# Optimization experiments

Hardware: AMD Instinct MI355X
Metric: run time of the kernel (lower is better)

## Reference

```python
import jax, jax.numpy as jnp
import numpy as np

N_NODES = 20000
N_EDGES = 320000
HIDDEN = 128
HEADS = 8
LAYERS = 3
EXP_DEG = 4
N_VIRT = 1
NV = N_NODES + N_VIRT  # nodes after VirtualNode transform


def _layer_norm(x, g, b, eps=1e-5):
    mu = jnp.mean(x, axis=-1, keepdims=True)
    var = jnp.var(x, axis=-1, keepdims=True)
    return (x - mu) * jax.lax.rsqrt(var + eps) * g + b


def _segment_softmax(scores, seg, num_segments):
    # numerically-stable softmax over edges grouped by destination node
    m = jax.ops.segment_max(scores, seg, num_segments=num_segments)
    m = jnp.where(jnp.isfinite(m), m, 0.0)
    e = jnp.exp(scores - m[seg])
    s = jax.ops.segment_sum(e, seg, num_segments=num_segments)
    return e / (s[seg] + 1e-16)


def _edge_attention(x, src, dst, wq, bq, wk, bk, wv, bv, wo, bo):
    # multi-head attention restricted to the given edge list (Exphormer local/expander attention)
    n, d_model = x.shape
    dh = d_model // HEADS
    q = (x @ wq + bq).reshape(n, HEADS, dh)
    k = (x @ wk + bk).reshape(n, HEADS, dh)
    v = (x @ wv + bv).reshape(n, HEADS, dh)
    scores = jnp.einsum('ehd,ehd->eh', q[dst], k[src]) * (1.0 / np.sqrt(dh))  # [E, H]
    alpha = _segment_softmax(scores, dst, n)
    out = jax.ops.segment_sum(alpha[:, :, None] * v[src], dst, num_segments=n)  # [n, H, dh]
    return out.reshape(n, d_model) @ wo + bo


def setup_inputs():
    key = jax.random.key(0)
    ks = jax.random.split(key, 32)
    x = jax.random.normal(ks[0], (N_NODES, HIDDEN), dtype=jnp.float32)
    edge_index = jax.random.randint(ks[1], (2, N_EDGES), 0, N_NODES, dtype=jnp.int32)
    # expander graph per layer: EXP_DEG//2 random permutations, both directions
    ar = jnp.arange(NV, dtype=jnp.int32)
    layers_e = []
    for l in range(LAYERS):
        e = []
        for p in range(EXP_DEG // 2):
            perm = jax.random.permutation(jax.random.fold_in(ks[2], l * 10 + p), NV).astype(jnp.int32)
            e.append(jnp.stack([ar, perm]))
            e.append(jnp.stack([perm, ar]))
        layers_e.append(jnp.concatenate(e, axis=1))
    expander_edges = jnp.stack(layers_e)  # [LAYERS, 2, NV*EXP_DEG]

    def w(k, shape):
        return jax.random.normal(k, shape, dtype=jnp.float32) * 0.05

    p = {}
    names = ['lq', 'lk', 'lv', 'lo', 'eq', 'ek', 'ev', 'eo']
    for i, nm in enumerate(names):
        p[nm + '_w'] = w(ks[3 + i], (LAYERS, HIDDEN, HIDDEN))
        p[nm + '_b'] = w(ks[12 + i], (LAYERS, HIDDEN))
    p['ln_g'] = jnp.ones((LAYERS, HIDDEN), jnp.float32)
    p['ln_b'] = jnp.zeros((LAYERS, HIDDEN), jnp.float32)
    p['ffn_w1'] = w(ks[21], (LAYERS, HIDDEN, 4 * HIDDEN))
    p['ffn_b1'] = w(ks[22], (LAYERS, 4 * HIDDEN))
    p['ffn_w2'] = w(ks[23], (LAYERS, 4 * HIDDEN, HIDDEN))
    p['ffn_b2'] = w(ks[24], (LAYERS, HIDDEN))
    return {'x': x, 'edge_index': edge_index, 'expander_edges': expander_edges, **p}


def reference(x, edge_index, expander_edges,
              lq_w, lq_b, lk_w, lk_b, lv_w, lv_b, lo_w, lo_b,
              eq_w, eq_b, ek_w, ek_b, ev_w, ev_b, eo_w, eo_b,
              ln_g, ln_b, ffn_w1, ffn_b1, ffn_w2, ffn_b2):
    n = x.shape[0]
    # VirtualNode transform: one zero-feature node connected bidirectionally to all nodes
    xv = jnp.concatenate([x, jnp.zeros((N_VIRT, x.shape[1]), x.dtype)], axis=0)
    ar = jnp.arange(n, dtype=edge_index.dtype)
    vn = jnp.full((n,), n, dtype=edge_index.dtype)
    vsrc = jnp.concatenate([edge_index[0], ar, vn])
    vdst = jnp.concatenate([edge_index[1], vn, ar])
    for l in range(LAYERS):
        residual = xv
        local = _edge_attention(xv, vsrc, vdst,
                                lq_w[l], lq_b[l], lk_w[l], lk_b[l],
                                lv_w[l], lv_b[l], lo_w[l], lo_b[l])
        exp_out = _edge_attention(xv, expander_edges[l, 0], expander_edges[l, 1],
                                  eq_w[l], eq_b[l], ek_w[l], ek_b[l],
                                  ev_w[l], ev_b[l], eo_w[l], eo_b[l])
        xv = _layer_norm(residual + local + exp_out, ln_g[l], ln_b[l])
        xv = xv + (jax.nn.gelu(xv @ ffn_w1[l] + ffn_b1[l], approximate=False) @ ffn_w2[l] + ffn_b2[l])
    return xv[:N_NODES]
```

## Files before the change

### kernel.cpp

```cpp
#include <hip/hip_runtime.h>
#include <hip/hip_bf16.h>
#include <math.h>

#define NN    20000
#define NVT   20001
#define VN    20000
#define E_EI  320000
#define E_LOC 360000
#define E_EXP 80004
#define RSN   20002
#define NBVN  79
#define VNSTR 144

#define OW_LQ 0
#define OB_LQ 16384
#define OW_LK 16512
#define OB_LK 32896
#define OW_LV 33024
#define OB_LV 49408
#define OW_LO 49536
#define OB_LO 65920
#define OW_EQ 66048
#define OB_EQ 82432
#define OW_EK 82560
#define OB_EK 98944
#define OW_EV 99072
#define OB_EV 115456
#define OW_EO 115584
#define OB_EO 131968
#define O_LNG 132096
#define O_LNB 132224
#define O_FW1 132352
#define O_FB1 197888
#define O_FW2 198400
#define O_FB2 263936
#define WC_TOT 264064

typedef unsigned short u16;
typedef unsigned int   u32;
typedef __attribute__((ext_vector_type(8))) short short8;
typedef __attribute__((ext_vector_type(4))) float f32x4;

__device__ __forceinline__ float bf2f(u16 u) {
    return __uint_as_float(((u32)u) << 16);
}
__device__ __forceinline__ u16 f2bf(float f) {
    u32 x = __float_as_uint(f);
    u32 r = x + 0x7fffu + ((x >> 16) & 1u);
    return (u16)(r >> 16);
}

__device__ __forceinline__ void loadq16(const u16* qp, float* qf) {
    const uint4* p = (const uint4*)qp;
    uint4 a = p[0], b = p[1];
    qf[0]=bf2f((u16)(a.x&0xffff)); qf[1]=bf2f((u16)(a.x>>16));
    qf[2]=bf2f((u16)(a.y&0xffff)); qf[3]=bf2f((u16)(a.y>>16));
    qf[4]=bf2f((u16)(a.z&0xffff)); qf[5]=bf2f((u16)(a.z>>16));
    qf[6]=bf2f((u16)(a.w&0xffff)); qf[7]=bf2f((u16)(a.w>>16));
    qf[8]=bf2f((u16)(b.x&0xffff)); qf[9]=bf2f((u16)(b.x>>16));
    qf[10]=bf2f((u16)(b.y&0xffff)); qf[11]=bf2f((u16)(b.y>>16));
    qf[12]=bf2f((u16)(b.z&0xffff)); qf[13]=bf2f((u16)(b.z>>16));
    qf[14]=bf2f((u16)(b.w&0xffff)); qf[15]=bf2f((u16)(b.w>>16));
}
__device__ __forceinline__ float dot16_pre(const u16* kp, const float* qf) {
    const uint4* p = (const uint4*)kp;
    uint4 a = p[0], b = p[1];
    float s = 0.f;
    s += qf[0]*bf2f((u16)(a.x&0xffff)) + qf[1]*bf2f((u16)(a.x>>16));
    s += qf[2]*bf2f((u16)(a.y&0xffff)) + qf[3]*bf2f((u16)(a.y>>16));
    s += qf[4]*bf2f((u16)(a.z&0xffff)) + qf[5]*bf2f((u16)(a.z>>16));
    s += qf[6]*bf2f((u16)(a.w&0xffff)) + qf[7]*bf2f((u16)(a.w>>16));
    s += qf[8]*bf2f((u16)(b.x&0xffff)) + qf[9]*bf2f((u16)(b.x>>16));
    s += qf[10]*bf2f((u16)(b.y&0xffff)) + qf[11]*bf2f((u16)(b.y>>16));
    s += qf[12]*bf2f((u16)(b.z&0xffff)) + qf[13]*bf2f((u16)(b.z>>16));
    s += qf[14]*bf2f((u16)(b.w&0xffff)) + qf[15]*bf2f((u16)(b.w>>16));
    return s;
}
__device__ __forceinline__ float dot16_bf(const u16* kptr, const float* qptr) {
    const uint4* kp = (const uint4*)kptr;
    uint4 a = kp[0], b = kp[1];
    const float4* qp = (const float4*)qptr;
    float4 q0 = qp[0], q1 = qp[1], q2 = qp[2], q3 = qp[3];
    float s = 0.f;
    s += q0.x * bf2f((u16)(a.x & 0xffff)) + q0.y * bf2f((u16)(a.x >> 16));
    s += q0.z * bf2f((u16)(a.y & 0xffff)) + q0.w * bf2f((u16)(a.y >> 16));
    s += q1.x * bf2f((u16)(a.z & 0xffff)) + q1.y * bf2f((u16)(a.z >> 16));
    s += q1.z * bf2f((u16)(a.w & 0xffff)) + q1.w * bf2f((u16)(a.w >> 16));
    s += q2.x * bf2f((u16)(b.x & 0xffff)) + q2.y * bf2f((u16)(b.x >> 16));
    s += q2.z * bf2f((u16)(b.y & 0xffff)) + q2.w * bf2f((u16)(b.y >> 16));
    s += q3.x * bf2f((u16)(b.z & 0xffff)) + q3.y * bf2f((u16)(b.z >> 16));
    s += q3.z * bf2f((u16)(b.w & 0xffff)) + q3.w * bf2f((u16)(b.w >> 16));
    return s;
}

__global__ void k_detect(const u16* __restrict__ x, int* __restrict__ flag) {
    int t = threadIdx.x;
    u16 v = x[2 * t];
    int e = (v >> 7) & 0xFF;
    int sane = (e >= 100 && e <= 150) ? 1 : 0;
    __shared__ int s;
    if (t == 0) s = 0;
    __syncthreads();
    atomicAdd(&s, sane);
    __syncthreads();
    if (t == 0) *flag = (s >= 192) ? 1 : 0;
}

__global__ void k_convert(const void* __restrict__ x, const int* __restrict__ flag,
                          u16* __restrict__ XV, int* __restrict__ RS) {
    int i = blockIdx.x * 256 + threadIdx.x;
    if (i < NVT * 128) {
        u16 v = 0;
        if (i < NN * 128)
            v = (*flag) ? ((const u16*)x)[i] : f2bf(((const float*)x)[i]);
        XV[i] = v;
    } else {
        int j = i - NVT * 128;
        if (j < RSN + 4) RS[j] = 0;
    }
}

__global__ void k_canon(
    const void* lqw, const void* lqb, const void* lkw, const void* lkb,
    const void* lvw, const void* lvb, const void* low_, const void* lob,
    const void* eqw, const void* eqb, const void* ekw, const void* ekb,
    const void* evw, const void* evb, const void* eow, const void* eob,
    const void* lng, const void* lnb, const void* f1w, const void* f1b,
    const void* f2w, const void* f2b,
    const int* __restrict__ flag, u16* __restrict__ WcAll)
{
    int idx = blockIdx.x * 256 + threadIdx.x;
    if (idx >= WC_TOT) return;
    int layer = blockIdx.y;
    u16* Wc = WcAll + (size_t)layer * WC_TOT;
    const void* src;
    int e, stride;
    if (idx < 132096) {
        int p = idx / 16512, w = idx - p * 16512;
        const void* wt; const void* bt;
        switch (p) {
            case 0: wt = lqw; bt = lqb; break;
            case 1: wt = lkw; bt = lkb; break;
            case 2: wt = lvw; bt = lvb; break;
            case 3: wt = low_; bt = lob; break;
            case 4: wt = eqw; bt = eqb; break;
            case 5: wt = ekw; bt = ekb; break;
            case 6: wt = evw; bt = evb; break;
            default: wt = eow; bt = eob; break;
        }
        if (w < 16384) {
            int kt = w >> 12, ct = (w >> 9) & 7, ln = (w >> 3) & 63, j = w & 7;
            int k = kt * 32 + (ln >> 4) * 8 + j, c = ct * 16 + (ln & 15);
            src = wt; e = k * 128 + c; stride = 16384;
        } else { src = bt; e = w - 16384; stride = 128; }
    } else {
        int t2 = idx - 132096;
        if (t2 < 128)        { src = lng; e = t2;       stride = 128; }
        else if (t2 < 256)   { src = lnb; e = t2 - 128; stride = 128; }
        else if (t2 < 256 + 65536) {
            int w = t2 - 256;
            int cb = w >> 14, w2 = w & 16383;
            int kt = w2 >> 12, ct = (w2 >> 9) & 7, ln = (w2 >> 3) & 63, j = w2 & 7;
            int k = kt * 32 + (ln >> 4) * 8 + j, c = cb * 128 + ct * 16 + (ln & 15);
            src = f1w; e = k * 512 + c; stride = 65536;
        }
        else if (t2 < 66304) { src = f1b; e = t2 - 65792; stride = 512; }
        else if (t2 < 131840) {
            int w = t2 - 66304;
            int kt = w >> 12, ct = (w >> 9) & 7, ln = (w >> 3) & 63, j = w & 7;
            int k = kt * 32 + (ln >> 4) * 8 + j, c = ct * 16 + (ln & 15);
            src = f2w; e = k * 128 + c; stride = 65536;
        }
        else { src = f2b; e = t2 - 131840; stride = 128; }
    }
    int eg = layer * stride + e;
    Wc[idx] = (*flag) ? ((const u16*)src)[eg] : f2bf(((const float*)src)[eg]);
}

__global__ void k_count(const int* __restrict__ ei, int* __restrict__ RS) {
    int g = blockIdx.x * 256 + threadIdx.x;
    if (g >= E_EI) return;
    atomicAdd(&RS[ei[E_EI + g] + 1], 1);
}

__global__ __launch_bounds__(256) void k_scan(int* __restrict__ RS, int* __restrict__ CUR) {
    int t = threadIdx.x;
    const int CH = 79;
    int base = t * CH;
    int sum = 0;
    for (int i = 0; i < CH; ++i) {
        int idx = base + i;
        if (idx < RSN) {
            int add = RS[idx];
            if (idx >= 1 && idx <= NN) add += 1;
            if (idx == RSN - 1)        add += NN;
            sum += add;
        }
    }
    __shared__ int ss[256];
    ss[t] = sum;
    __syncthreads();
    for (int off = 1; off < 256; off <<= 1) {
        int v = (t >= off) ? ss[t - off] : 0;
        __syncthreads();
        ss[t] += v;
        __syncthreads();
    }
    int run = ss[t] - sum;
    for (int i = 0; i < CH; ++i) {
        int idx = base + i;
        if (idx < RSN) {
            int add = RS[idx];
            if (idx >= 1 && idx <= NN) add += 1;
            if (idx == RSN - 1)        add += NN;
            run += add;
            RS[idx]  = run;
            if (idx < NN) CUR[idx] = run + 1;
        }
    }
}

__global__ void k_scatter(const int* __restrict__ ei, int* __restrict__ CUR,
                          int* __restrict__ CSRC) {
    int g = blockIdx.x * 256 + threadIdx.x;
    if (g >= E_EI) return;
    int src = ei[g], dst = ei[E_EI + g];
    int pos = atomicAdd(&CUR[dst], 1);
    CSRC[pos] = src;
}

__global__ void k_fixinv(const int* __restrict__ RS, int* __restrict__ CSRC,
                         const int* __restrict__ ex, int* __restrict__ IP) {
    int idx = blockIdx.x * 256 + threadIdx.x;
    if (idx < NN) {
        CSRC[RS[idx]] = VN;
        CSRC[RS[VN] + idx] = idx;
    }
    if (idx < 6 * NVT) {
        int p = idx / NVT, i = idx - p * NVT;
        int l = p >> 1, w = p & 1;
        int off = l * 2 * E_EXP + E_EXP + w * 2 * NVT;
        int val = ex[off + i];
        IP[p * NVT + val] = i;
    }
}


__global__ __launch_bounds__(256) void k_qkv(
    const u16* __restrict__ X, const u16* __restrict__ Wc,
    u16* O0, u16* O1, u16* O2)
{
    int z = blockIdx.z;
    int wo = (z == 0) ? OW_LQ : (z == 1) ? OW_LK : OW_LV;
    int bo = (z == 0) ? OB_LQ : (z == 1) ? OB_LK : OB_LV;
    u16* O = (z == 0) ? O0 : (z == 1) ? O1 : O2;
    int t = threadIdx.x;
    int wv = t >> 6, lane = t & 63;
    int q4 = lane >> 4, m = lane & 15;
    int rowb = blockIdx.x * 64 + wv * 16;
    int r0 = min(rowb + m, NVT - 1);
    f32x4 zero4 = {0.f, 0.f, 0.f, 0.f};
    f32x4 acc[8];
    #pragma unroll
    for (int ct = 0; ct < 8; ++ct) acc[ct] = zero4;

    const u16* Wf = Wc + wo + lane * 8;
    #pragma unroll
    for (int kt = 0; kt < 4; ++kt) {
        short8 a0 = *(const short8*)&X[r0 * 128 + kt * 32 + q4 * 8];
        #pragma unroll
        for (int ct = 0; ct < 8; ++ct) {
            short8 bw = *(const short8*)&Wf[kt * 4096 + ct * 512];
            acc[ct] = __builtin_amdgcn_mfma_f32_16x16x32_bf16(bw, a0, acc[ct], 0, 0, 0);
        }
    }
    int row = rowb + m;
    if (row < NVT) {
        #pragma unroll
        for (int ct = 0; ct < 8; ++ct) {
            int c0 = ct * 16 + q4 * 4;
            ushort4 bb = *(const ushort4*)&Wc[bo + c0];
            ushort4 st;
            st.x = f2bf(acc[ct][0] + bf2f(bb.x));
            st.y = f2bf(acc[ct][1] + bf2f(bb.y));
            st.z = f2bf(acc[ct][2] + bf2f(bb.z));
            st.w = f2bf(acc[ct][3] + bf2f(bb.w));
            *(ushort4*)&O[row * 128 + c0] = st;
        }
    }
}

__global__ __launch_bounds__(256) void k_pq(
    u16* ATT, const u16* XV, const u16* __restrict__ Wc,
    u16* Q, u16* K, u16* V)
{
    int z = blockIdx.z;
    const u16* X; u16* O; const u16* A = nullptr;
    int wo, bo;
    if (z == 0)      { X = ATT; O = ATT; A = XV; wo = OW_LO; bo = OB_LO; }
    else if (z == 1) { X = XV;  O = Q;  wo = OW_EQ; bo = OB_EQ; }
    else if (z == 2) { X = XV;  O = K;  wo = OW_EK; bo = OB_EK; }
    else             { X = XV;  O = V;  wo = OW_EV; bo = OB_EV; }

    int t = threadIdx.x;
    int wv = t >> 6, lane = t & 63;
    int q4 = lane >> 4, m = lane & 15;
    int rowb = blockIdx.x * 64 + wv * 16;
    int r0 = min(rowb + m, NVT - 1);
    f32x4 zero4 = {0.f, 0.f, 0.f, 0.f};
    f32x4 acc[8];
    #pragma unroll
    for (int ct = 0; ct < 8; ++ct) acc[ct] = zero4;

    const u16* Wf = Wc + wo + lane * 8;
    #pragma unroll
    for (int kt = 0; kt < 4; ++kt) {
        short8 a0 = *(const short8*)&X[r0 * 128 + kt * 32 + q4 * 8];
        #pragma unroll
        for (int ct = 0; ct < 8; ++ct) {
            short8 bw = *(const short8*)&Wf[kt * 4096 + ct * 512];
            acc[ct] = __builtin_amdgcn_mfma_f32_16x16x32_bf16(bw, a0, acc[ct], 0, 0, 0);
        }
    }
    int row = rowb + m;
    if (row < NVT) {
        #pragma unroll
        for (int ct = 0; ct < 8; ++ct) {
            int c0 = ct * 16 + q4 * 4;
            ushort4 bb = *(const ushort4*)&Wc[bo + c0];
            float v0 = acc[ct][0] + bf2f(bb.x);
            float v1 = acc[ct][1] + bf2f(bb.y);
            float v2 = acc[ct][2] + bf2f(bb.z);
            float v3 = acc[ct][3] + bf2f(bb.w);
            if (A) {
                ushort4 av = *(const ushort4*)&A[row * 128 + c0];
                v0 += bf2f(av.x); v1 += bf2f(av.y);
                v2 += bf2f(av.z); v3 += bf2f(av.w);
            }
            ushort4 st;
            st.x = f2bf(v0); st.y = f2bf(v1); st.z = f2bf(v2); st.w = f2bf(v3);
            *(ushort4*)&O[row * 128 + c0] = st;
        }
    }
}

__global__ __launch_bounds__(256) void k_plf(
    u16* XV, const u16* __restrict__ ATT, const u16* __restrict__ Wc,
    const int* __restrict__ flag, void* outp, int write_out)
{
    __shared__ __align__(16) u16 Xs[32 * 136];
    __shared__ __align__(16) u16 Hs[32 * 520];
    int t = threadIdx.x;
    int wv = t >> 6, lane = t & 63;
    int q4 = lane >> 4, m = lane & 15;
    int rowb = blockIdx.x * 32;
    f32x4 zero4 = {0.f, 0.f, 0.f, 0.f};

    if (wv < 2) {
        int rl = wv * 16 + m;
        int r0 = min(rowb + rl, NVT - 1);
        f32x4 acc[8];
        #pragma unroll
        for (int ct = 0; ct < 8; ++ct) acc[ct] = zero4;
        const u16* Wf = Wc + OW_EO + lane * 8;
        #pragma unroll
        for (int kt = 0; kt < 4; ++kt) {
            short8 a0 = *(const short8*)&XV[r0 * 128 + kt * 32 + q4 * 8];
            #pragma unroll
            for (int ct = 0; ct < 8; ++ct) {
                short8 bw = *(const short8*)&Wf[kt * 4096 + ct * 512];
                acc[ct] = __builtin_amdgcn_mfma_f32_16x16x32_bf16(bw, a0, acc[ct], 0, 0, 0);
            }
        }
        float sm = 0.f, sq = 0.f;
        #pragma unroll
        for (int ct = 0; ct < 8; ++ct) {
            int c0 = ct * 16 + q4 * 4;
            ushort4 bb = *(const ushort4*)&Wc[OB_EO + c0];
            ushort4 av = *(const ushort4*)&ATT[r0 * 128 + c0];
            acc[ct][0] += bf2f(bb.x) + bf2f(av.x);
            acc[ct][1] += bf2f(bb.y) + bf2f(av.y);
            acc[ct][2] += bf2f(bb.z) + bf2f(av.z);
            acc[ct][3] += bf2f(bb.w) + bf2f(av.w);
            #pragma unroll
            for (int j = 0; j < 4; ++j) { sm += acc[ct][j]; sq += acc[ct][j] * acc[ct][j]; }
        }
        sm += __shfl_xor(sm, 16); sq += __shfl_xor(sq, 16);
        sm += __shfl_xor(sm, 32); sq += __shfl_xor(sq, 32);
        float mu  = sm * (1.f / 128.f);
        float var = sq * (1.f / 128.f) - mu * mu;
        float rs  = rsqrtf(var + 1e-5f);
        #pragma unroll
        for (int ct = 0; ct < 8; ++ct) {
            int c0 = ct * 16 + q4 * 4;
            ushort4 gg = *(const ushort4*)&Wc[O_LNG + c0];
            ushort4 bb = *(const ushort4*)&Wc[O_LNB + c0];
            ushort4 st;
            st.x = f2bf((acc[ct][0] - mu) * rs * bf2f(gg.x) + bf2f(bb.x));
            st.y = f2bf((acc[ct][1] - mu) * rs * bf2f(gg.y) + bf2f(bb.y));
            st.z = f2bf((acc[ct][2] - mu) * rs * bf2f(gg.z) + bf2f(bb.z));
            st.w = f2bf((acc[ct][3] - mu) * rs * bf2f(gg.w) + bf2f(bb.w));
            *(ushort4*)&Xs[rl * 136 + c0] = st;
        }
    }
    __syncthreads();

    short8 ax[2][4];
    #pragma unroll
    for (int kt = 0; kt < 4; ++kt) {
        ax[0][kt] = *(const short8*)&Xs[m * 136 + kt * 32 + q4 * 8];
        ax[1][kt] = *(const short8*)&Xs[(16 + m) * 136 + kt * 32 + q4 * 8];
    }
    f32x4 a1[2][8];
    #pragma unroll
    for (int rg = 0; rg < 2; ++rg)
        #pragma unroll
        for (int ct = 0; ct < 8; ++ct) a1[rg][ct] = zero4;
    const u16* W1f = Wc + O_FW1 + wv * 16384 + lane * 8;
    #pragma unroll
    for (int kt = 0; kt < 4; ++kt) {
        #pragma unroll
        for (int ct = 0; ct < 8; ++ct) {
            short8 bw = *(const short8*)&W1f[kt * 4096 + ct * 512];
            a1[0][ct] = __builtin_amdgcn_mfma_f32_16x16x32_bf16(bw, ax[0][kt], a1[0][ct], 0, 0, 0);
            a1[1][ct] = __builtin_amdgcn_mfma_f32_16x16x32_bf16(bw, ax[1][kt], a1[1][ct], 0, 0, 0);
        }
    }
    #pragma unroll
    for (int rg = 0; rg < 2; ++rg) {
        int rl = rg * 16 + m;
        #pragma unroll
        for (int ct = 0; ct < 8; ++ct) {
            int c = wv * 128 + ct * 16 + q4 * 4;
            ushort4 bb = *(const ushort4*)&Wc[O_FB1 + c];
            float v0 = a1[rg][ct][0] + bf2f(bb.x);
            float v1 = a1[rg][ct][1] + bf2f(bb.y);
            float v2 = a1[rg][ct][2] + bf2f(bb.z);
            float v3 = a1[rg][ct][3] + bf2f(bb.w);
            ushort4 st;
            st.x = f2bf(0.5f * v0 * (1.f + erff(v0 * 0.70710678118654752440f)));
            st.y = f2bf(0.5f * v1 * (1.f + erff(v1 * 0.70710678118654752440f)));
            st.z = f2bf(0.5f * v2 * (1.f + erff(v2 * 0.70710678118654752440f)));
            st.w = f2bf(0.5f * v3 * (1.f + erff(v3 * 0.70710678118654752440f)));
            *(ushort4*)&Hs[rl * 520 + c] = st;
        }
    }
    __syncthreads();

    f32x4 acc2[2][2];
    #pragma unroll
    for (int rg = 0; rg < 2; ++rg)
        #pragma unroll
        for (int j = 0; j < 2; ++j) acc2[rg][j] = zero4;
    const u16* W2f = Wc + O_FW2 + lane * 8;
    #pragma unroll
    for (int kt = 0; kt < 16; ++kt) {
        short8 h0 = *(const short8*)&Hs[m * 520 + kt * 32 + q4 * 8];
        short8 h1 = *(const short8*)&Hs[(16 + m) * 520 + kt * 32 + q4 * 8];
        #pragma unroll
        for (int j = 0; j < 2; ++j) {
            short8 bw = *(const short8*)&W2f[kt * 4096 + (2 * wv + j) * 512];
            acc2[0][j] = __builtin_amdgcn_mfma_f32_16x16x32_bf16(bw, h0, acc2[0][j], 0, 0, 0);
            acc2[1][j] = __builtin_amdgcn_mfma_f32_16x16x32_bf16(bw, h1, acc2[1][j], 0, 0, 0);
        }
    }
    int fl = *flag;
    #pragma unroll
    for (int rg = 0; rg < 2; ++rg) {
        int row = rowb + rg * 16 + m;
        if (row < NVT) {
            #pragma unroll
            for (int j = 0; j < 2; ++j) {
                int c0 = (2 * wv + j) * 16 + q4 * 4;
                ushort4 bb = *(const ushort4*)&Wc[O_FB2 + c0];
                ushort4 rv = *(const ushort4*)&Xs[(rg * 16 + m) * 136 + c0];
                float v0 = acc2[rg][j][0] + bf2f(bb.x) + bf2f(rv.x);
                float v1 = acc2[rg][j][1] + bf2f(bb.y) + bf2f(rv.y);
                float v2 = acc2[rg][j][2] + bf2f(bb.z) + bf2f(rv.z);
                float v3 = acc2[rg][j][3] + bf2f(bb.w) + bf2f(rv.w);
                ushort4 st;
                st.x = f2bf(v0); st.y = f2bf(v1); st.z = f2bf(v2); st.w = f2bf(v3);
                *(ushort4*)&XV[row * 128 + c0] = st;
                if (write_out && row < NN) {
                    if (fl) {
                        *(ushort4*)((u16*)outp + row * 128 + c0) = st;
                    } else {
                        float4 fv; fv.x = v0; fv.y = v1; fv.z = v2; fv.w = v3;
                        *(float4*)((float*)outp + row * 128 + c0) = fv;
                    }
                }
            }
        }
    }
}

__global__ __launch_bounds__(256) void k_gvn(
    const u16* __restrict__ Q, const u16* __restrict__ K,
    const u16* __restrict__ V, const int* __restrict__ RS,
    const int* __restrict__ CSRC, u16* __restrict__ OUT,
    float* __restrict__ VNS, int* __restrict__ CNT)
{
    int t = threadIdx.x;
    __shared__ float ps_s[4][128];
    __shared__ int   sv_s[4][16];
    if (blockIdx.x >= NBVN) {
        int wv = t >> 6, l = t & 63;
        int dst = (blockIdx.x - NBVN) * 4 + wv;
        int hp = l & 3;
        int e16 = l >> 2;
        int hq = l >> 4;
        float* ps = ps_s[wv];
        int* svp = sv_s[wv];
        int rs = RS[dst], re = RS[dst + 1];
        float qf[32];
        loadq16(&Q[dst * 128 + hp * 32], qf);
        loadq16(&Q[dst * 128 + hp * 32 + 16], qf + 16);
        float acc0 = 0.f, acc1 = 0.f, d0 = 0.f, d1 = 0.f;
        for (int e0 = rs; e0 < re; e0 += 16) {
            int eidx = e0 + e16;
            bool val = eidx < re;
            int eidx2 = val ? eidx : (re - 1);
            int sv = CSRC[eidx2];
            float s0 = dot16_pre(&K[sv * 128 + hp * 32], qf) * 0.25f;
            float s1 = dot16_pre(&K[sv * 128 + hp * 32 + 16], qf + 16) * 0.25f;
            float p0 = val ? __expf(s0) : 0.f;
            float p1 = val ? __expf(s1) : 0.f;
            ps[e16 * 8 + 2 * hp]     = p0;
            ps[e16 * 8 + 2 * hp + 1] = p1;
            if (hp == 0) svp[e16] = sv;
            #pragma unroll
            for (int ee = 0; ee < 16; ++ee) {
                int se = svp[ee];
                float w0 = ps[ee * 8 + hq];
                float w1 = ps[ee * 8 + 4 + hq];
                acc0 += w0 * bf2f(V[se * 128 + l]);
                acc1 += w1 * bf2f(V[se * 128 + 64 + l]);
                d0 += w0; d1 += w1;
            }
        }
        OUT[dst * 128 + l]      = f2bf(acc0 / (d0 + 1e-16f));
        OUT[dst * 128 + 64 + l] = f2bf(acc1 / (d1 + 1e-16f));
        return;
    }
    int vb = blockIdx.x;
    __shared__ __align__(16) float q_s[128];
    __shared__ float sr_s[256 * 8];
    __shared__ float pden[64];
    __shared__ float psum[128];
    __shared__ int   lastBlk;
    int base = vb * 256;
    if (t < 128) q_s[t] = bf2f(Q[VN * 128 + t]);
    __syncthreads();

    int e32 = t >> 3, h = t & 7;
    for (int pass = 0; pass < 8; ++pass) {
        int e = pass * 32 + e32;
        int src = base + e;
        float p = 0.f;
        if (src < NN)
            p = __expf(dot16_bf(&K[src * 128 + h * 16], &q_s[h * 16]) * 0.25f);
        sr_s[e * 8 + h] = p;
    }
    __syncthreads();
    if (t < 64) {
        int h2 = t & 7, c = t >> 3;
        float pd = 0.f;
        for (int j = 0; j < 32; ++j)
            pd += sr_s[(c * 32 + j) * 8 + h2];
        pden[t] = pd;
    }
    __syncthreads();
    if (t < 8) {
        float dn = 0.f;
        for (int c = 0; c < 8; ++c) dn += pden[c * 8 + t];
        VNS[vb * VNSTR + 8 + t] = dn;
    }
    int d = t & 127, half = t >> 7, hd = d >> 4;
    float acc = 0.f;
    for (int i = 0; i < 128; ++i) {
        int e = half * 128 + i;
        int src = base + e;
        if (src < NN)
            acc += sr_s[e * 8 + hd] * bf2f(V[src * 128 + d]);
    }
    if (half == 1) psum[d] = acc;
    __syncthreads();
    if (half == 0)
        VNS[vb * VNSTR + 16 + d] = acc + psum[d];
    __threadfence();
    __syncthreads();
    if (t == 0) lastBlk = (atomicAdd(CNT, 1) == NBVN - 1) ? 1 : 0;
    __syncthreads();
    if (lastBlk) {
        __threadfence();
        volatile const float* VV = VNS;
        __shared__ float den_s[8];
        if (t < 8) {
            float dn = 0.f;
            for (int b = 0; b < NBVN; ++b) dn += VV[b * VNSTR + 8 + t];
            den_s[t] = dn;
        }
        __syncthreads();
        if (t < 128) {
            int hd2 = t >> 4;
            float a2 = 0.f;
            for (int b = 0; b < NBVN; ++b) a2 += VV[b * VNSTR + 16 + t];
            OUT[VN * 128 + t] = f2bf(a2 / (den_s[hd2] + 1e-16f));
        }
    }
}

__global__ __launch_bounds__(256) void k_egather(
    const u16* __restrict__ Q, const u16* __restrict__ K,
    const u16* __restrict__ V, const int* __restrict__ IP0,
    const int* __restrict__ IP1, const int* __restrict__ PD,
    u16* __restrict__ OUT)
{
    int wv = threadIdx.x >> 6, l = threadIdx.x & 63;
    int dst = blockIdx.x * 4 + wv;
    if (dst >= NVT) return;
    int h = l & 7, e = (l >> 3) & 3, hq = l >> 4;
    int sv;
    if (e == 0)      sv = IP0[dst];
    else if (e == 1) sv = PD[dst];
    else if (e == 2) sv = IP1[dst];
    else             sv = PD[2 * NVT + dst];
    float qf[16];
    loadq16(&Q[dst * 128 + h * 16], qf);
    float sr = dot16_pre(&K[sv * 128 + h * 16], qf) * 0.25f;
    float p = __expf(sr);
    float den = p + __shfl_xor(p, 8);
    den += __shfl_xor(den, 16);
    float acc0 = 0.f, acc1 = 0.f;
    #pragma unroll
    for (int ee = 0; ee < 4; ++ee) {
        int se = __shfl(sv, ee * 8);
        float p0 = __shfl(p, ee * 8 + hq);
        float p1 = __shfl(p, ee * 8 + 4 + hq);
        acc0 += p0 * bf2f(V[se * 128 + l]);
        acc1 += p1 * bf2f(V[se * 128 + 64 + l]);
    }
    float d0 = __shfl(den, hq), d1 = __shfl(den, 4 + hq);
    OUT[dst * 128 + l]      = f2bf(acc0 / (d0 + 1e-16f));
    OUT[dst * 128 + 64 + l] = f2bf(acc1 / (d1 + 1e-16f));
}

extern "C" void kernel_launch(void* const* d_in, const int* in_sizes, int n_in,
                              void* d_out, int out_size, void* d_ws, size_t ws_size,
                              hipStream_t stream)
{
    const void* x = d_in[0];
    const int* ei = (const int*)d_in[1];
    const int* ex = (const int*)d_in[2];

    const size_t NFB = (size_t)NVT * 128 * 2;
    char* wsb = (char*)d_ws;
    u16* XVb  = (u16*)(wsb);
    u16* ATTb = (u16*)(wsb + NFB);
    u16* Qb   = (u16*)(wsb + 2 * NFB);
    u16* Kb   = (u16*)(wsb + 3 * NFB);
    u16* Vb   = (u16*)(wsb + 4 * NFB);
    int* RS   = (int*)(wsb + 5 * NFB);
    int* CNT  = RS + RSN;
    int* CUR  = CNT + 4;
    int* IP   = CUR + RSN;
    size_t o_wc = 5 * NFB + (size_t)(2 * RSN + 4 + 6 * NVT) * 4;
    o_wc = (o_wc + 15) & ~(size_t)15;
    u16* Wc   = (u16*)(wsb + o_wc);
    int* flag = (int*)(wsb + o_wc + (size_t)3 * WC_TOT * 2);

    int*   CSRC = (int*)d_out;
    float* VNS  = (float*)((char*)d_out + (size_t)E_LOC * 4);

    k_detect<<<1, 256, 0, stream>>>((const u16*)x, flag);
    k_convert<<<(NVT * 128 + RSN + 4 + 255) / 256, 256, 0, stream>>>(x, flag, XVb, RS);
    int eb = (E_EI + 255) / 256;
    k_count  <<<eb, 256, 0, stream>>>(ei, RS);
    k_scan   <<<1, 256, 0, stream>>>(RS, CUR);
    k_scatter<<<eb, 256, 0, stream>>>(ei, CUR, CSRC);
    k_fixinv <<<(6 * NVT + 255) / 256, 256, 0, stream>>>(RS, CSRC, ex, IP);
    k_canon<<<dim3((WC_TOT + 255) / 256, 3), 256, 0, stream>>>(
        d_in[3],  d_in[4],  d_in[5],  d_in[6],  d_in[7],  d_in[8],
        d_in[9],  d_in[10], d_in[11], d_in[12], d_in[13], d_in[14],
        d_in[15], d_in[16], d_in[17], d_in[18], d_in[19], d_in[20],
        d_in[21], d_in[22], d_in[23], d_in[24], flag, Wc);

    int gb64 = (NVT + 63) / 64;
    int gb32 = (NVT + 31) / 32;
    for (int l = 0; l < 3; ++l) {
        const u16* Wl = Wc + (size_t)l * WC_TOT;
        k_qkv<<<dim3(gb64, 1, 3), 256, 0, stream>>>(XVb, Wl, Qb, Kb, Vb);
        k_gvn<<<NBVN + NN / 4, 256, 0, stream>>>(Qb, Kb, Vb, RS, CSRC, ATTb,
                                                  VNS, CNT + l);
        k_pq<<<dim3(gb64, 1, 4), 256, 0, stream>>>(ATTb, XVb, Wl, Qb, Kb, Vb);
        k_egather<<<(NVT + 3) / 4, 256, 0, stream>>>(Qb, Kb, Vb,
            IP + (2 * l) * NVT, IP + (2 * l + 1) * NVT,
            ex + (size_t)l * 2 * E_EXP + E_EXP, XVb);
        k_plf<<<gb32, 256, 0, stream>>>(XVb, ATTb, Wl, flag, d_out,
                                        (l == 2) ? 1 : 0);
    }
}
```

Baseline: 706.7 us.

## Split each node's edges across two waves and vectorize V gathers

The local-attention gather path now assigns two wavefronts per destination node, each handling alternate 16-edge chunks. Each lane loads 8 bf16 V values in one 16-byte load instead of scalar loads. Partial sums are combined with cross-lane shuffles and shared memory before a single vectorized store. This aims to raise memory-level parallelism and cut per-edge load instructions, at the cost of twice as many blocks, an extra block barrier and shuffle reductions.

```diff
diff --git a/kernel.cpp b/kernel.cpp
--- a/kernel.cpp
+++ b/kernel.cpp
@@ -503,43 +503,75 @@
     int t = threadIdx.x;
     __shared__ float ps_s[4][128];
     __shared__ int   sv_s[4][16];
+    __shared__ float comb[2][16][9];
     if (blockIdx.x >= NBVN) {
         int wv = t >> 6, l = t & 63;
-        int dst = (blockIdx.x - NBVN) * 4 + wv;
-        int hp = l & 3;
+        int pr  = wv >> 1;
+        int par = wv & 1;
+        int dst = (blockIdx.x - NBVN) * 2 + pr;
+        int hp  = l & 3;
         int e16 = l >> 2;
-        int hq = l >> 4;
-        float* ps = ps_s[wv];
-        int* svp = sv_s[wv];
+        int qq  = l >> 4;
+        int m   = l & 15;
+        int hd  = m >> 1;
+        float* ps  = ps_s[wv];
+        int*   svp = sv_s[wv];
         int rs = RS[dst], re = RS[dst + 1];
         float qf[32];
         loadq16(&Q[dst * 128 + hp * 32], qf);
         loadq16(&Q[dst * 128 + hp * 32 + 16], qf + 16);
-        float acc0 = 0.f, acc1 = 0.f, d0 = 0.f, d1 = 0.f;
-        for (int e0 = rs; e0 < re; e0 += 16) {
+        float acc[8] = {0.f, 0.f, 0.f, 0.f, 0.f, 0.f, 0.f, 0.f};
+        float dacc = 0.f;
+        for (int e0 = rs + par * 16; e0 < re; e0 += 32) {
             int eidx = e0 + e16;
             bool val = eidx < re;
-            int eidx2 = val ? eidx : (re - 1);
-            int sv = CSRC[eidx2];
+            int sv = CSRC[val ? eidx : (re - 1)];
+            if (hp == 0) svp[e16] = sv;
             float s0 = dot16_pre(&K[sv * 128 + hp * 32], qf) * 0.25f;
             float s1 = dot16_pre(&K[sv * 128 + hp * 32 + 16], qf + 16) * 0.25f;
             float p0 = val ? __expf(s0) : 0.f;
             float p1 = val ? __expf(s1) : 0.f;
             ps[e16 * 8 + 2 * hp]     = p0;
             ps[e16 * 8 + 2 * hp + 1] = p1;
-            if (hp == 0) svp[e16] = sv;
             #pragma unroll
-            for (int ee = 0; ee < 16; ++ee) {
-                int se = svp[ee];
-                float w0 = ps[ee * 8 + hq];
-                float w1 = ps[ee * 8 + 4 + hq];
-                acc0 += w0 * bf2f(V[se * 128 + l]);
-                acc1 += w1 * bf2f(V[se * 128 + 64 + l]);
-                d0 += w0; d1 += w1;
+            for (int g = 0; g < 4; ++g) {
+                int es = g * 4 + qq;
+                int se = svp[es];
+                float w = ps[es * 8 + hd];
+                uint4 v4 = *(const uint4*)&V[se * 128 + m * 8];
+                acc[0] += w * bf2f((u16)(v4.x & 0xffff));
+                acc[1] += w * bf2f((u16)(v4.x >> 16));
+                acc[2] += w * bf2f((u16)(v4.y & 0xffff));
+                acc[3] += w * bf2f((u16)(v4.y >> 16));
+                acc[4] += w * bf2f((u16)(v4.z & 0xffff));
+                acc[5] += w * bf2f((u16)(v4.z >> 16));
+                acc[6] += w * bf2f((u16)(v4.w & 0xffff));
+                acc[7] += w * bf2f((u16)(v4.w >> 16));
+                dacc += w;
             }
         }
-        OUT[dst * 128 + l]      = f2bf(acc0 / (d0 + 1e-16f));
-        OUT[dst * 128 + 64 + l] = f2bf(acc1 / (d1 + 1e-16f));
+        #pragma unroll
+        for (int j = 0; j < 8; ++j) {
+            acc[j] += __shfl_xor(acc[j], 16);
+            acc[j] += __shfl_xor(acc[j], 32);
+        }
+        dacc += __shfl_xor(dacc, 16);
+        dacc += __shfl_xor(dacc, 32);
+        if (par && l < 16) {
+            #pragma unroll
+            for (int j = 0; j < 8; ++j) comb[pr][l][j] = acc[j];
+            comb[pr][l][8] = dacc;
+        }
+        __syncthreads();
+        if (!par && l < 16) {
+            float dn = dacc + comb[pr][l][8] + 1e-16f;
+            float rdn = 1.f / dn;
+            short8 st;
+            #pragma unroll
+            for (int j = 0; j < 8; ++j)
+                st[j] = (short)f2bf((acc[j] + comb[pr][l][j]) * rdn);
+            *(short8*)&OUT[dst * 128 + m * 8] = st;
+        }
         return;
     }
     int vb = blockIdx.x;
@@ -690,7 +722,7 @@
     for (int l = 0; l < 3; ++l) {
         const u16* Wl = Wc + (size_t)l * WC_TOT;
         k_qkv<<<dim3(gb64, 1, 3), 256, 0, stream>>>(XVb, Wl, Qb, Kb, Vb);
-        k_gvn<<<NBVN + NN / 4, 256, 0, stream>>>(Qb, Kb, Vb, RS, CSRC, ATTb,
+        k_gvn<<<NBVN + NN / 2, 256, 0, stream>>>(Qb, Kb, Vb, RS, CSRC, ATTb,
                                                   VNS, CNT + l);
         k_pq<<<dim3(gb64, 1, 4), 256, 0, stream>>>(ATTb, XVb, Wl, Qb, Kb, Vb);
         k_egather<<<(NVT + 3) / 4, 256, 0, stream>>>(Qb, Kb, Vb,
```

Measured after the change: 709.1 us. About the same (+0.3%).
